# Performance work log

Measured on AMD Instinct MI355X. Metric: run time of the kernel, lower is better.

Reference implementation:

```python
import jax, jax.numpy as jnp
import numpy as np

BS, N, L, H, E, W, K = 32, 512, 4096, 256, 64, 8, 9
NE = 2048            # edges per graph
CIN = H + 2 * E + W  # pc1 input channels
CS = K // 2          # center slice start
LC = L - (K - 1)     # valid-conv output length
EPS = 1e-5


def setup_inputs() -> dict:
    key = jax.random.key(0)
    ks = jax.random.split(key, 12)
    s = 0.05
    d = {}
    d["x"] = jax.random.normal(ks[0], (BS, N, H), jnp.float32)
    d["edge_feat"] = jax.random.normal(ks[1], (BS, NE, E), jnp.float32)
    d["walk_nodes"] = jax.random.randint(ks[2], (BS, L), 0, N - 1)
    d["walk_edges"] = jax.random.randint(ks[3], (BS, L - 1), 0, NE)
    d["encodings"] = jax.random.normal(ks[4], (BS, W, L), jnp.float32)
    d["ln_g"] = jnp.ones((H,), jnp.float32)
    d["ln_b"] = jnp.zeros((H,), jnp.float32)
    d["pc1_w"] = jax.random.normal(ks[5], (2 * H, CIN), jnp.float32) * s
    d["pc1_b"] = jnp.zeros((2 * H,), jnp.float32)
    d["dc_w"] = jax.random.normal(ks[6], (H, K), jnp.float32) * s
    d["bn_g"] = jnp.ones((H,), jnp.float32)
    d["bn_b"] = jnp.zeros((H,), jnp.float32)
    d["pc2_w"] = jax.random.normal(ks[7], (H, H), jnp.float32) * s
    d["pc2_b"] = jnp.zeros((H,), jnp.float32)
    d["mlp_w1"] = jax.random.normal(ks[8], (H, H), jnp.float32) * s
    d["bn2_g"] = jnp.ones((H,), jnp.float32)
    d["bn2_b"] = jnp.zeros((H,), jnp.float32)
    d["mlp_w2"] = jax.random.normal(ks[9], (H, H), jnp.float32) * s
    return d


def reference(x, edge_feat, walk_nodes, walk_edges, encodings,
              ln_g, ln_b, pc1_w, pc1_b, dc_w, bn_g, bn_b,
              pc2_w, pc2_b, mlp_w1, bn2_g, bn2_b, mlp_w2):
    # LayerNorm over hidden dim
    mu = x.mean(-1, keepdims=True)
    var = x.var(-1, keepdims=True)
    xn = (x - mu) * jax.lax.rsqrt(var + EPS) * ln_g + ln_b

    vn = xn[:, 0]  # [BS, H]

    # gather walk node features: x[batch, walk_nodes+1] -> [BS, H, L]
    xg = jnp.take_along_axis(xn, (walk_nodes + 1)[:, :, None], axis=1)
    xg = xg.transpose(0, 2, 1)

    # gather walk edge features -> [BS, E, L-1], pad to in/out channels of len L
    we = jnp.take_along_axis(edge_feat, walk_edges[:, :, None], axis=1).transpose(0, 2, 1)
    pad = jnp.zeros((BS, E, 1), xg.dtype)
    we_i = jnp.concatenate([pad, we], axis=2)
    we_o = jnp.concatenate([we, pad], axis=2)

    h = jnp.concatenate([xg, we_i, we_o, encodings], axis=1)  # [BS, CIN, L]

    # pointwise conv 1 + GLU
    h = jnp.einsum('oc,bcl->bol', pc1_w, h) + pc1_b[None, :, None]
    out, gate = jnp.split(h, 2, axis=1)
    h = out * jax.nn.sigmoid(gate)  # [BS, H, L]

    # depthwise conv, VALID -> [BS, H, LC]
    h = jax.lax.conv_general_dilated(
        h, dc_w[:, None, :], window_strides=(1,), padding='VALID',
        feature_group_count=H, dimension_numbers=('NCH', 'OIH', 'NCH'))

    # BatchNorm1d (training mode, biased var over batch+length)
    m = h.mean((0, 2))
    v = h.var((0, 2))
    h = (h - m[None, :, None]) * jax.lax.rsqrt(v + EPS)[None, :, None] \
        * bn_g[None, :, None] + bn_b[None, :, None]

    # Swish + pointwise conv 2
    h = h * jax.nn.sigmoid(h)
    h = jnp.einsum('oc,bcl->bol', pc2_w, h) + pc2_b[None, :, None]
    h = h.transpose(0, 2, 1)  # [BS, LC, H]

    # scatter_mean over center nodes into n-1 real-node slots
    center = jax.lax.dynamic_slice_in_dim(walk_nodes, CS, LC, axis=1)  # [BS, LC]
    flat_idx = (center + jnp.arange(BS, dtype=center.dtype)[:, None] * (N - 1)).reshape(-1)
    sums = jax.ops.segment_sum(h.reshape(BS * LC, H), flat_idx, num_segments=BS * (N - 1))
    cnt = jax.ops.segment_sum(jnp.ones((BS * LC,), h.dtype), flat_idx, num_segments=BS * (N - 1))
    node_out = (sums / jnp.maximum(cnt, 1.0)[:, None]).reshape(BS, N - 1, H)

    # virtual node MLP: Linear -> BN -> ReLU -> Linear
    z = (vn + node_out.sum(1)) @ mlp_w1.T
    m2 = z.mean(0)
    v2 = z.var(0)
    z = (z - m2) * jax.lax.rsqrt(v2 + EPS) * bn2_g + bn2_b
    z = jax.nn.relu(z) @ mlp_w2.T
    vn_out = z[:, None]  # [BS, 1, H]

    return jnp.concatenate([vn_out, node_out + vn_out], axis=1)  # [BS, N, H]
```

## Files before the change

### kernel.cpp

```cpp
#include <hip/hip_runtime.h>
#include <hip/hip_bf16.h>

typedef __hip_bfloat16 bf16;
typedef __attribute__((ext_vector_type(8))) short short8v;
typedef __attribute__((ext_vector_type(4))) float f32x4;

#define BS 32
#define NN 512
#define LL 4096
#define HH 256
#define EE 64
#define WW 8
#define KK 9
#define NE 2048
#define CIN 392
#define KP 416
#define FS 424
#define FS2 264
#define LC 4088
#define NM1 511
#define CR 128
#define K2M 128
#define K5M 64

__device__ __forceinline__ float b2f(bf16 v) { return __bfloat162float(v); }
__device__ __forceinline__ float bfr(unsigned short u) {
    union { unsigned int i; float f; } cv; cv.i = ((unsigned int)u) << 16; return cv.f;
}
__device__ __forceinline__ unsigned short f2b(float v) {
    return __builtin_bit_cast(unsigned short, __float2bfloat16(v));
}
__device__ __forceinline__ unsigned int pack2(float a, float b) {
    return (unsigned int)f2b(a) | ((unsigned int)f2b(b) << 16);
}
__device__ __forceinline__ float sigm(float x) {
    return __builtin_amdgcn_rcpf(1.f + __expf(-x));
}

__global__ void k0_all(const float* __restrict__ pc1w, const float* __restrict__ pc2w,
                       const float* __restrict__ edge, unsigned short* __restrict__ wb,
                       unsigned short* __restrict__ w2b, unsigned short* __restrict__ eb) {
    size_t i = (size_t)blockIdx.x * 256 + threadIdx.x;
    eb[i] = f2b(edge[i]);
    if (i < (size_t)512 * KP) {
        int row = (int)(i / KP), c = (int)(i % KP);
        wb[i] = (c < CIN) ? f2b(pc1w[(size_t)row * CIN + c]) : 0;
    }
    if (i < (size_t)HH * HH) w2b[i] = f2b(pc2w[i]);
}

__global__ void k1_layernorm(const float* __restrict__ x, const float* __restrict__ ln_g,
                             const float* __restrict__ ln_b, unsigned short* __restrict__ xnb,
                             float* __restrict__ acc) {
    int b = blockIdx.y, n = blockIdx.x, t = threadIdx.x;
    size_t base = ((size_t)(b * NN + n)) * HH;
    float v = x[base + t];
    __shared__ float s1[4], s2[4], mv[2];
    float a = v, q = v * v;
    #pragma unroll
    for (int o = 32; o > 0; o >>= 1) { a += __shfl_down(a, o, 64); q += __shfl_down(q, o, 64); }
    if ((t & 63) == 0) { s1[t >> 6] = a; s2[t >> 6] = q; }
    __syncthreads();
    if (t == 0) {
        float sa = s1[0] + s1[1] + s1[2] + s1[3];
        float sq = s2[0] + s2[1] + s2[2] + s2[3];
        float mean = sa * (1.0f / 256.0f);
        float var = sq * (1.0f / 256.0f) - mean * mean;
        mv[0] = mean; mv[1] = rsqrtf(var + 1e-5f);
    }
    __syncthreads();
    float outv = (v - mv[0]) * mv[1] * ln_g[t] + ln_b[t];
    xnb[base + t] = f2b(outv);
    if (n == 0) acc[b * HH + t] = outv;
}

__global__ void kb1_count(const int* __restrict__ wn, int* __restrict__ count) {
    int b = blockIdx.y, l = blockIdx.x * 256 + threadIdx.x;
    if (l < LC) atomicAdd(&count[b * NM1 + wn[b * LL + l + (KK / 2)]], 1);
}

__global__ void kb2_scan(const int* __restrict__ count, int* __restrict__ offs,
                         int* __restrict__ cursor) {
    int b = blockIdx.x, t = threadIdx.x;
    __shared__ int ps[256];
    int c0 = (2 * t < NM1)     ? count[b * NM1 + 2 * t]     : 0;
    int c1 = (2 * t + 1 < NM1) ? count[b * NM1 + 2 * t + 1] : 0;
    int pair = c0 + c1;
    ps[t] = pair;
    __syncthreads();
    for (int o = 1; o < 256; o <<= 1) {
        int add = (t >= o) ? ps[t - o] : 0;
        __syncthreads();
        ps[t] += add;
        __syncthreads();
    }
    int ex = ps[t] - pair;
    offs[b * 512 + 2 * t] = ex;
    offs[b * 512 + 2 * t + 1] = ex + c0;
    if (2 * t < NM1)     cursor[b * NM1 + 2 * t]     = ex;
    if (2 * t + 1 < NM1) cursor[b * NM1 + 2 * t + 1] = ex + c0;
}

__global__ void kb3_fill(const int* __restrict__ wn, int* __restrict__ cursor,
                         int* __restrict__ bins) {
    int b = blockIdx.y, l = blockIdx.x * 256 + threadIdx.x;
    if (l < LC) {
        int c = wn[b * LL + l + (KK / 2)];
        int slot = atomicAdd(&cursor[b * NM1 + c], 1);
        bins[b * LC + slot] = l;
    }
}

__global__ void __launch_bounds__(512, 2)
k2_mfma(const unsigned short* __restrict__ xnb, const unsigned short* __restrict__ edgeb,
        const int* __restrict__ wn, const int* __restrict__ we,
        const float* __restrict__ enc, const unsigned short* __restrict__ wb,
        const float* __restrict__ pc1_b, unsigned short* __restrict__ h1) {
    __shared__ __align__(16) unsigned short smem[K2M * FS];
    __shared__ int rown[K2M], ein[K2M], eout[K2M];
    int b = blockIdx.y, l0 = blockIdx.x * K2M, t = threadIdx.x;
    int lane = t & 63, wv = t >> 6;
    int l15 = lane & 15, lr = (lane >> 4) & 3, koff = lr * 8;
    int isG = wv >> 2;
    int c0 = isG * 256 + (wv & 3) * 64;
    const unsigned short* wr = wb + ((size_t)(c0 + l15)) * KP + koff;

    short8v b0[4], b1[4];
    #pragma unroll
    for (int n = 0; n < 4; ++n) b0[n] = *(const short8v*)(wr + (size_t)n * 16 * KP);

    if (t < K2M) {
        int l = l0 + t;
        rown[t] = wn[b * LL + l] + 1;
        ein[t]  = (l > 0)      ? we[b * (LL - 1) + l - 1] : -1;
        eout[t] = (l < LL - 1) ? we[b * (LL - 1) + l]     : -1;
    }
    __syncthreads();

    for (int i = t; i < K2M * 32; i += 512) {
        int r = i >> 5, c = (i & 31) * 8;
        *(uint4*)&smem[r * FS + c] =
            *(const uint4*)(xnb + ((size_t)(b * NN + rown[r])) * HH + c);
    }
    for (int i = t; i < K2M * 16; i += 512) {
        int r = i >> 4, q = i & 15;
        int idx = (q < 8) ? ein[r] : eout[r];
        uint4 v = {0u, 0u, 0u, 0u};
        if (idx >= 0)
            v = *(const uint4*)(edgeb + ((size_t)(b * NE + idx)) * EE + (q & 7) * 8);
        *(uint4*)&smem[r * FS + HH + q * 8] = v;
    }
    for (int i = t; i < K2M * 5; i += 512) {
        int r = i / 5, q = i % 5;
        uint4 v = {0u, 0u, 0u, 0u};
        if (q == 0) {
            const float* ep = enc + (size_t)b * WW * LL + (l0 + r);
            v.x = pack2(ep[0], ep[LL]);          v.y = pack2(ep[2 * LL], ep[3 * LL]);
            v.z = pack2(ep[4 * LL], ep[5 * LL]); v.w = pack2(ep[6 * LL], ep[7 * LL]);
        }
        *(uint4*)&smem[r * FS + (HH + 2 * EE) + q * 8] = v;
    }
    __syncthreads();

    f32x4 acc[8][4];
    #pragma unroll
    for (int m = 0; m < 8; ++m)
        #pragma unroll
        for (int n = 0; n < 4; ++n) acc[m][n] = (f32x4){0.f, 0.f, 0.f, 0.f};

    const unsigned short* arow = &smem[l15 * FS + koff];

    #pragma unroll 1
    for (int p = 0; p < 6; ++p) {
        int kk = 2 * p;
        #pragma unroll
        for (int n = 0; n < 4; ++n)
            b1[n] = *(const short8v*)(wr + (size_t)n * 16 * KP + (kk + 1) * 32);
        {
            short8v a[8];
            #pragma unroll
            for (int m = 0; m < 8; ++m)
                a[m] = *(const short8v*)(arow + (size_t)m * 16 * FS + kk * 32);
            #pragma unroll
            for (int m = 0; m < 8; ++m)
                #pragma unroll
                for (int n = 0; n < 4; ++n)
                    acc[m][n] = __builtin_amdgcn_mfma_f32_16x16x32_bf16(a[m], b0[n], acc[m][n], 0, 0, 0);
        }
        #pragma unroll
        for (int n = 0; n < 4; ++n)
            b0[n] = *(const short8v*)(wr + (size_t)n * 16 * KP + (kk + 2) * 32);
        {
            short8v a[8];
            #pragma unroll
            for (int m = 0; m < 8; ++m)
                a[m] = *(const short8v*)(arow + (size_t)m * 16 * FS + (kk + 1) * 32);
            #pragma unroll
            for (int m = 0; m < 8; ++m)
                #pragma unroll
                for (int n = 0; n < 4; ++n)
                    acc[m][n] = __builtin_amdgcn_mfma_f32_16x16x32_bf16(a[m], b1[n], acc[m][n], 0, 0, 0);
        }
    }
    {
        short8v a[8];
        #pragma unroll
        for (int m = 0; m < 8; ++m)
            a[m] = *(const short8v*)(arow + (size_t)m * 16 * FS + 12 * 32);
        #pragma unroll
        for (int m = 0; m < 8; ++m)
            #pragma unroll
            for (int n = 0; n < 4; ++n)
                acc[m][n] = __builtin_amdgcn_mfma_f32_16x16x32_bf16(a[m], b0[n], acc[m][n], 0, 0, 0);
    }

    float bias[4];
    #pragma unroll
    for (int n = 0; n < 4; ++n) bias[n] = pc1_b[c0 + n * 16 + l15];

    __syncthreads();
    unsigned short* glu = smem;
    int cb = (wv & 3) * 64 + l15;
    if (isG) {
        #pragma unroll
        for (int m = 0; m < 8; ++m)
            #pragma unroll
            for (int n = 0; n < 4; ++n)
                #pragma unroll
                for (int r = 0; r < 4; ++r) {
                    int pos = m * 16 + lr * 4 + r;
                    glu[pos * FS2 + cb + n * 16] = f2b(acc[m][n][r] + bias[n]);
                }
    }
    __syncthreads();
    if (!isG) {
        #pragma unroll
        for (int m = 0; m < 8; ++m)
            #pragma unroll
            for (int n = 0; n < 4; ++n)
                #pragma unroll
                for (int r = 0; r < 4; ++r) {
                    int pos = m * 16 + lr * 4 + r;
                    float g = bfr(glu[pos * FS2 + cb + n * 16]);
                    float o = acc[m][n][r] + bias[n];
                    glu[pos * FS2 + cb + n * 16] = f2b(o * sigm(g));
                }
    }
    __syncthreads();
    for (int i = t; i < K2M * 32; i += 512) {
        int r = i >> 5, c = (i & 31) * 8;
        *(uint4*)(h1 + ((size_t)(b * LL) + l0 + r) * HH + c) = *(const uint4*)&glu[r * FS2 + c];
    }
}

__global__ void k3f_conv_stats(const unsigned short* __restrict__ h1, const float* __restrict__ dc_w,
                               unsigned short* __restrict__ h2, float* __restrict__ bnsum,
                               float* __restrict__ bnsumsq) {
    __shared__ float sr[4][HH], qr[4][HH];
    int b = blockIdx.y, l0 = blockIdx.x * CR, t = threadIdx.x;
    int g = t >> 6, c4 = (t & 63) * 4;
    int rows_all = min(CR, LC - l0);
    int r0 = g * (CR / 4);
    int r1 = min(r0 + CR / 4, rows_all);

    float wk[4][KK];
    #pragma unroll
    for (int j = 0; j < 4; ++j)
        #pragma unroll
        for (int k = 0; k < KK; ++k) wk[j][k] = dc_w[(c4 + j) * KK + k];

    float s[4] = {0.f, 0.f, 0.f, 0.f}, q[4] = {0.f, 0.f, 0.f, 0.f};
    if (r0 < r1) {
        const unsigned short* src = h1 + ((size_t)b * LL + l0 + r0) * HH + c4;
        float w[KK][4];
        float nxt[4];
        #pragma unroll
        for (int k = 0; k < KK - 1; ++k) {
            uint2 v = *(const uint2*)(src + (size_t)k * HH);
            w[k][0] = bfr((unsigned short)(v.x & 0xffffu)); w[k][1] = bfr((unsigned short)(v.x >> 16));
            w[k][2] = bfr((unsigned short)(v.y & 0xffffu)); w[k][3] = bfr((unsigned short)(v.y >> 16));
        }
        {
            uint2 v = *(const uint2*)(src + (size_t)(KK - 1) * HH);
            nxt[0] = bfr((unsigned short)(v.x & 0xffffu)); nxt[1] = bfr((unsigned short)(v.x >> 16));
            nxt[2] = bfr((unsigned short)(v.y & 0xffffu)); nxt[3] = bfr((unsigned short)(v.y >> 16));
        }
        for (int i = r0; i < r1; ++i) {
            #pragma unroll
            for (int j = 0; j < 4; ++j) w[KK - 1][j] = nxt[j];
            if (i + 1 < r1) {
                uint2 v = *(const uint2*)(src + (size_t)(i - r0 + KK) * HH);
                nxt[0] = bfr((unsigned short)(v.x & 0xffffu)); nxt[1] = bfr((unsigned short)(v.x >> 16));
                nxt[2] = bfr((unsigned short)(v.y & 0xffffu)); nxt[3] = bfr((unsigned short)(v.y >> 16));
            }
            float o[4];
            #pragma unroll
            for (int j = 0; j < 4; ++j) {
                float v = 0.f;
                #pragma unroll
                for (int k = 0; k < KK; ++k) v += w[k][j] * wk[j][k];
                o[j] = v;
                s[j] += v; q[j] += v * v;
            }
            uint2 ov;
            ov.x = pack2(o[0], o[1]); ov.y = pack2(o[2], o[3]);
            *(uint2*)(h2 + ((size_t)b * LC + l0 + i) * HH + c4) = ov;
            #pragma unroll
            for (int k = 0; k < KK - 1; ++k)
                #pragma unroll
                for (int j = 0; j < 4; ++j) w[k][j] = w[k + 1][j];
        }
    }
    #pragma unroll
    for (int j = 0; j < 4; ++j) { sr[g][c4 + j] = s[j]; qr[g][c4 + j] = q[j]; }
    __syncthreads();
    float ss = sr[0][t] + sr[1][t] + sr[2][t] + sr[3][t];
    float qq = qr[0][t] + qr[1][t] + qr[2][t] + qr[3][t];
    atomicAdd(&bnsum[t], ss);
    atomicAdd(&bnsumsq[t], qq);
}

__global__ void k4b_finalize(const float* __restrict__ bnsum, const float* __restrict__ bnsumsq,
                             const float* __restrict__ bn_g, const float* __restrict__ bn_b,
                             float* __restrict__ bnscale, float* __restrict__ bnshift) {
    int c = threadIdx.x;
    const float M = (float)(BS * LC);
    float mean = bnsum[c] / M;
    float var = bnsumsq[c] / M - mean * mean;
    float rstd = rsqrtf(var + 1e-5f);
    float sc = rstd * bn_g[c];
    bnscale[c] = sc;
    bnshift[c] = bn_b[c] - mean * sc;
}

__global__ void __launch_bounds__(256, 3)
k5_mfma(const unsigned short* __restrict__ h2, const float* __restrict__ bnscale,
        const float* __restrict__ bnshift, const unsigned short* __restrict__ w2b,
        const float* __restrict__ pc2_b, unsigned short* __restrict__ h3) {
    __shared__ __align__(16) unsigned short smem[K5M * FS2];
    __shared__ float scl[HH], shl[HH];
    int b = blockIdx.y, l0 = blockIdx.x * K5M, t = threadIdx.x;
    int lane = t & 63, wv = t >> 6;
    int l15 = lane & 15, lr = (lane >> 4) & 3, koff = lr * 8;
    int c0 = wv * 64;
    const unsigned short* wrow = w2b + ((size_t)(c0 + l15)) * HH + koff;

    short8v b0[4], b1[4];
    #pragma unroll
    for (int n = 0; n < 4; ++n) b0[n] = *(const short8v*)(wrow + (size_t)n * 16 * HH);

    scl[t] = bnscale[t];
    shl[t] = bnshift[t];
    __syncthreads();

    for (int i = t; i < K5M * 32; i += 256) {
        int r = i >> 5, c = (i & 31) * 8;
        int l = l0 + r;
        uint4 out = {0u, 0u, 0u, 0u};
        if (l < LC) {
            uint4 v = *(const uint4*)(h2 + ((size_t)b * LC + l) * HH + c);
            unsigned int vv[4] = {v.x, v.y, v.z, v.w};
            unsigned int oo[4];
            #pragma unroll
            for (int j = 0; j < 4; ++j) {
                float f0 = bfr((unsigned short)(vv[j] & 0xffffu));
                float f1 = bfr((unsigned short)(vv[j] >> 16));
                float a0 = f0 * scl[c + 2 * j]     + shl[c + 2 * j];
                float a1 = f1 * scl[c + 2 * j + 1] + shl[c + 2 * j + 1];
                a0 = a0 * sigm(a0);
                a1 = a1 * sigm(a1);
                oo[j] = pack2(a0, a1);
            }
            out.x = oo[0]; out.y = oo[1]; out.z = oo[2]; out.w = oo[3];
        }
        *(uint4*)&smem[r * FS2 + c] = out;
    }
    __syncthreads();

    f32x4 acc[4][4];
    #pragma unroll
    for (int m = 0; m < 4; ++m)
        #pragma unroll
        for (int n = 0; n < 4; ++n) acc[m][n] = (f32x4){0.f, 0.f, 0.f, 0.f};

    const unsigned short* arow = &smem[l15 * FS2 + koff];

    #pragma unroll 1
    for (int p = 0; p < 4; ++p) {
        int kk = 2 * p;
        #pragma unroll
        for (int n = 0; n < 4; ++n)
            b1[n] = *(const short8v*)(wrow + (size_t)n * 16 * HH + (kk + 1) * 32);
        {
            short8v a[4];
            #pragma unroll
            for (int m = 0; m < 4; ++m)
                a[m] = *(const short8v*)(arow + (size_t)m * 16 * FS2 + kk * 32);
            #pragma unroll
            for (int m = 0; m < 4; ++m)
                #pragma unroll
                for (int n = 0; n < 4; ++n)
                    acc[m][n] = __builtin_amdgcn_mfma_f32_16x16x32_bf16(a[m], b0[n], acc[m][n], 0, 0, 0);
        }
        if (p < 3) {
            #pragma unroll
            for (int n = 0; n < 4; ++n)
                b0[n] = *(const short8v*)(wrow + (size_t)n * 16 * HH + (kk + 2) * 32);
        }
        {
            short8v a[4];
            #pragma unroll
            for (int m = 0; m < 4; ++m)
                a[m] = *(const short8v*)(arow + (size_t)m * 16 * FS2 + (kk + 1) * 32);
            #pragma unroll
            for (int m = 0; m < 4; ++m)
                #pragma unroll
                for (int n = 0; n < 4; ++n)
                    acc[m][n] = __builtin_amdgcn_mfma_f32_16x16x32_bf16(a[m], b1[n], acc[m][n], 0, 0, 0);
        }
    }

    int chb = c0 + l15;
    float bias[4];
    #pragma unroll
    for (int n = 0; n < 4; ++n) bias[n] = pc2_b[chb + n * 16];

    __syncthreads();
    #pragma unroll
    for (int m = 0; m < 4; ++m)
        #pragma unroll
        for (int n = 0; n < 4; ++n)
            #pragma unroll
            for (int r = 0; r < 4; ++r) {
                int pos = m * 16 + lr * 4 + r;
                smem[pos * FS2 + chb + n * 16] = f2b(acc[m][n][r] + bias[n]);
            }
    __syncthreads();
    for (int i = t; i < K5M * 32; i += 256) {
        int r = i >> 5, c = (i & 31) * 8;
        int l = l0 + r;
        if (l < LC)
            *(uint4*)(h3 + ((size_t)b * LC + l) * HH + c) = *(const uint4*)&smem[r * FS2 + c];
    }
}

__global__ void k6_gather(const unsigned short* __restrict__ h3, const int* __restrict__ offs,
                          const int* __restrict__ bins, float* __restrict__ node_out) {
    int bn = blockIdx.x;
    int b = bn / NM1, n = bn % NM1, t = threadIdx.x;
    int s = offs[b * 512 + n], e = offs[b * 512 + n + 1];
    float sum = 0.f;
    for (int i = s; i < e; ++i) {
        int l = bins[b * LC + i];
        sum += bfr(h3[((size_t)b * LC + l) * HH + t]);
    }
    float inv = 1.f / (float)max(e - s, 1);
    node_out[(size_t)bn * HH + t] = sum * inv;
}

__global__ void k6b_accsum(const float* __restrict__ node_out, float* __restrict__ acc) {
    int b = blockIdx.y, g = blockIdx.x, t = threadIdx.x;
    int n0 = g * 32, n1 = min(n0 + 32, NM1);
    float s = 0.f;
    for (int n = n0; n < n1; ++n) s += node_out[((size_t)b * NM1 + n) * HH + t];
    atomicAdd(&acc[b * HH + t], s);
}

__global__ void k7_mlp1(const float* __restrict__ acc, const float* __restrict__ w1,
                        float* __restrict__ z) {
    int b = blockIdx.x, t = threadIdx.x;
    __shared__ float a[HH];
    a[t] = acc[b * HH + t];
    __syncthreads();
    const float* w = w1 + (size_t)t * HH;
    float s = 0.f;
    for (int c = 0; c < HH; ++c) s += w[c] * a[c];
    z[b * HH + t] = s;
}

__global__ void k8_bn2(float* __restrict__ z, const float* __restrict__ g2,
                       const float* __restrict__ b2v) {
    int t = threadIdx.x;
    float vals[BS];
    float m = 0.f, q = 0.f;
    for (int b = 0; b < BS; ++b) {
        float v = z[b * HH + t];
        vals[b] = v; m += v; q += v * v;
    }
    m *= (1.0f / BS);
    q = q * (1.0f / BS) - m * m;
    float rstd = rsqrtf(q + 1e-5f);
    float sc = rstd * g2[t];
    float sh = b2v[t] - m * sc;
    for (int b = 0; b < BS; ++b) z[b * HH + t] = fmaxf(vals[b] * sc + sh, 0.f);
}

__global__ void k9_mlp2(const float* __restrict__ z, const float* __restrict__ w2,
                        float* __restrict__ vnout) {
    int b = blockIdx.x, t = threadIdx.x;
    __shared__ float a[HH];
    a[t] = z[b * HH + t];
    __syncthreads();
    const float* w = w2 + (size_t)t * HH;
    float s = 0.f;
    for (int c = 0; c < HH; ++c) s += w[c] * a[c];
    vnout[b * HH + t] = s;
}

__global__ void k10_out(const float* __restrict__ vnout, const float* __restrict__ node_out,
                        float* __restrict__ out) {
    int bn = blockIdx.x;
    int b = bn >> 9, n = bn & (NN - 1), t = threadIdx.x;
    float vo = vnout[b * HH + t];
    float v = (n == 0) ? vo : node_out[((size_t)b * NM1 + (n - 1)) * HH + t] + vo;
    out[(size_t)bn * HH + t] = v;
}

extern "C" void kernel_launch(void* const* d_in, const int* in_sizes, int n_in,
                              void* d_out, int out_size, void* d_ws, size_t ws_size,
                              hipStream_t stream) {
    const float* x     = (const float*)d_in[0];
    const float* edge  = (const float*)d_in[1];
    const int*   wn    = (const int*)d_in[2];
    const int*   we    = (const int*)d_in[3];
    const float* enc   = (const float*)d_in[4];
    const float* ln_g  = (const float*)d_in[5];
    const float* ln_b  = (const float*)d_in[6];
    const float* pc1_w = (const float*)d_in[7];
    const float* pc1_b = (const float*)d_in[8];
    const float* dc_w  = (const float*)d_in[9];
    const float* bn_g  = (const float*)d_in[10];
    const float* bn_b  = (const float*)d_in[11];
    const float* pc2_w = (const float*)d_in[12];
    const float* pc2_b = (const float*)d_in[13];
    const float* w1    = (const float*)d_in[14];
    const float* g2    = (const float*)d_in[15];
    const float* b2v   = (const float*)d_in[16];
    const float* w2    = (const float*)d_in[17];

    char* ws = (char*)d_ws;
    unsigned short* xnb   = (unsigned short*)(ws + 0);
    unsigned short* wbf   = (unsigned short*)(ws + 8388608);
    unsigned short* h1    = (unsigned short*)(ws + 8814592);
    unsigned short* h3    = h1;
    unsigned short* h2    = (unsigned short*)(ws + 75923456);
    float* node_out = (float*)(ws + 142901248);
    unsigned short* edgeb = (unsigned short*)(ws + 142901248);
    int*   count   = (int*)(ws + 159645696);
    float* bnsum   = (float*)(ws + 159711104);
    float* bnsumsq = (float*)(ws + 159712128);
    float* acc     = (float*)(ws + 159713152);
    float* bnscale = (float*)(ws + 159745920);
    float* bnshift = (float*)(ws + 159746944);
    float* z       = (float*)(ws + 159747968);
    float* vnout   = (float*)(ws + 159780736);
    unsigned short* w2b = (unsigned short*)(ws + 159813504);
    int*   offs    = (int*)(ws + 159944576);
    int*   cursor  = (int*)(ws + 160010112);
    int*   bins    = (int*)(ws + 160075520);

    hipMemsetAsync(ws + 159645696, 0, 67456, stream);

    k0_all<<<(BS * NE * EE) / 256, 256, 0, stream>>>(pc1_w, pc2_w, edge, wbf, w2b, edgeb);
    k1_layernorm<<<dim3(NN, BS), 256, 0, stream>>>(x, ln_g, ln_b, xnb, acc);
    kb1_count<<<dim3(16, BS), 256, 0, stream>>>(wn, count);
    kb2_scan<<<BS, 256, 0, stream>>>(count, offs, cursor);
    kb3_fill<<<dim3(16, BS), 256, 0, stream>>>(wn, cursor, bins);
    k2_mfma<<<dim3(LL / K2M, BS), 512, 0, stream>>>(xnb, edgeb, wn, we, enc, wbf, pc1_b, h1);
    k3f_conv_stats<<<dim3((LC + CR - 1) / CR, BS), 256, 0, stream>>>(h1, dc_w, h2, bnsum, bnsumsq);
    k4b_finalize<<<1, 256, 0, stream>>>(bnsum, bnsumsq, bn_g, bn_b, bnscale, bnshift);
    k5_mfma<<<dim3((LC + K5M - 1) / K5M, BS), 256, 0, stream>>>(h2, bnscale, bnshift, w2b, pc2_b, h3);
    k6_gather<<<BS * NM1, 256, 0, stream>>>(h3, offs, bins, node_out);
    k6b_accsum<<<dim3(16, BS), 256, 0, stream>>>(node_out, acc);
    k7_mlp1<<<BS, 256, 0, stream>>>(acc, w1, z);
    k8_bn2<<<1, 256, 0, stream>>>(z, g2, b2v);
    k9_mlp2<<<BS, 256, 0, stream>>>(z, w2, vnout);
    k10_out<<<BS * NN, 256, 0, stream>>>(vnout, node_out, (float*)d_out);
}
```

Baseline: 297.0 us.

## Fuse binning kernels into one LDS kernel and restructure GLU GEMM tiling

The three binning kernels (count, scan, fill) are merged into a single per-batch kernel that does its histogram and cursor atomics in shared memory, which removes two launches and the global count/cursor buffers and shrinks the memset. The pc1 GEMM kernel now uses 64-row tiles and 256 threads, and each wave computes both the output and gate columns for the same 64 channels. The GLU can then be applied directly from registers, with no round trip through shared memory and no extra barrier. The cost is twice as many blocks, each loading its own copy of the weight B-fragments, and more accumulator registers per wave. The binning kernel now runs on only 32 blocks.

Result: faster. 290.7 us (-2.1%).

```diff
diff --git a/kernel.cpp b/kernel.cpp
--- a/kernel.cpp
+++ b/kernel.cpp
@@ -20,7 +20,7 @@
 #define LC 4088
 #define NM1 511
 #define CR 128
-#define K2M 128
+#define K2M 64
 #define K5M 64
 
 __device__ __forceinline__ float b2f(bf16 v) { return __bfloat162float(v); }
@@ -74,17 +74,19 @@
     if (n == 0) acc[b * HH + t] = outv;
 }
 
-__global__ void kb1_count(const int* __restrict__ wn, int* __restrict__ count) {
-    int b = blockIdx.y, l = blockIdx.x * 256 + threadIdx.x;
-    if (l < LC) atomicAdd(&count[b * NM1 + wn[b * LL + l + (KK / 2)]], 1);
-}
-
-__global__ void kb2_scan(const int* __restrict__ count, int* __restrict__ offs,
-                         int* __restrict__ cursor) {
+__global__ void kb_all(const int* __restrict__ wn, int* __restrict__ offs,
+                       int* __restrict__ bins) {
+    __shared__ int cnt[NM1];
+    __shared__ int cur[NM1];
+    __shared__ int ps[256];
     int b = blockIdx.x, t = threadIdx.x;
-    __shared__ int ps[256];
-    int c0 = (2 * t < NM1)     ? count[b * NM1 + 2 * t]     : 0;
-    int c1 = (2 * t + 1 < NM1) ? count[b * NM1 + 2 * t + 1] : 0;
+    for (int i = t; i < NM1; i += 256) cnt[i] = 0;
+    __syncthreads();
+    for (int l = t; l < LC; l += 256)
+        atomicAdd(&cnt[wn[b * LL + l + (KK / 2)]], 1);
+    __syncthreads();
+    int c0 = (2 * t < NM1)     ? cnt[2 * t]     : 0;
+    int c1 = (2 * t + 1 < NM1) ? cnt[2 * t + 1] : 0;
     int pair = c0 + c1;
     ps[t] = pair;
     __syncthreads();
@@ -97,21 +99,17 @@
     int ex = ps[t] - pair;
     offs[b * 512 + 2 * t] = ex;
     offs[b * 512 + 2 * t + 1] = ex + c0;
-    if (2 * t < NM1)     cursor[b * NM1 + 2 * t]     = ex;
-    if (2 * t + 1 < NM1) cursor[b * NM1 + 2 * t + 1] = ex + c0;
-}
-
-__global__ void kb3_fill(const int* __restrict__ wn, int* __restrict__ cursor,
-                         int* __restrict__ bins) {
-    int b = blockIdx.y, l = blockIdx.x * 256 + threadIdx.x;
-    if (l < LC) {
+    if (2 * t < NM1)     cur[2 * t]     = ex;
+    if (2 * t + 1 < NM1) cur[2 * t + 1] = ex + c0;
+    __syncthreads();
+    for (int l = t; l < LC; l += 256) {
         int c = wn[b * LL + l + (KK / 2)];
-        int slot = atomicAdd(&cursor[b * NM1 + c], 1);
+        int slot = atomicAdd(&cur[c], 1);
         bins[b * LC + slot] = l;
     }
 }
 
-__global__ void __launch_bounds__(512, 2)
+__global__ void __launch_bounds__(256, 2)
 k2_mfma(const unsigned short* __restrict__ xnb, const unsigned short* __restrict__ edgeb,
         const int* __restrict__ wn, const int* __restrict__ we,
         const float* __restrict__ enc, const unsigned short* __restrict__ wb,
@@ -121,13 +119,16 @@
     int b = blockIdx.y, l0 = blockIdx.x * K2M, t = threadIdx.x;
     int lane = t & 63, wv = t >> 6;
     int l15 = lane & 15, lr = (lane >> 4) & 3, koff = lr * 8;
-    int isG = wv >> 2;
-    int c0 = isG * 256 + (wv & 3) * 64;
-    const unsigned short* wr = wb + ((size_t)(c0 + l15)) * KP + koff;
-
-    short8v b0[4], b1[4];
-    #pragma unroll
-    for (int n = 0; n < 4; ++n) b0[n] = *(const short8v*)(wr + (size_t)n * 16 * KP);
+    int c0 = wv * 64;
+    const unsigned short* wrO = wb + ((size_t)(c0 + l15)) * KP + koff;
+    const unsigned short* wrG = wb + ((size_t)(HH + c0 + l15)) * KP + koff;
+
+    short8v bo0[4], bg0[4], bo1[4], bg1[4];
+    #pragma unroll
+    for (int n = 0; n < 4; ++n) {
+        bo0[n] = *(const short8v*)(wrO + (size_t)n * 16 * KP);
+        bg0[n] = *(const short8v*)(wrG + (size_t)n * 16 * KP);
+    }
 
     if (t < K2M) {
         int l = l0 + t;
@@ -137,12 +138,12 @@
     }
     __syncthreads();
 
-    for (int i = t; i < K2M * 32; i += 512) {
+    for (int i = t; i < K2M * 32; i += 256) {
         int r = i >> 5, c = (i & 31) * 8;
         *(uint4*)&smem[r * FS + c] =
             *(const uint4*)(xnb + ((size_t)(b * NN + rown[r])) * HH + c);
     }
-    for (int i = t; i < K2M * 16; i += 512) {
+    for (int i = t; i < K2M * 16; i += 256) {
         int r = i >> 4, q = i & 15;
         int idx = (q < 8) ? ein[r] : eout[r];
         uint4 v = {0u, 0u, 0u, 0u};
@@ -150,7 +151,7 @@
             v = *(const uint4*)(edgeb + ((size_t)(b * NE + idx)) * EE + (q & 7) * 8);
         *(uint4*)&smem[r * FS + HH + q * 8] = v;
     }
-    for (int i = t; i < K2M * 5; i += 512) {
+    for (int i = t; i < K2M * 5; i += 256) {
         int r = i / 5, q = i % 5;
         uint4 v = {0u, 0u, 0u, 0u};
         if (q == 0) {
@@ -162,11 +163,11 @@
     }
     __syncthreads();
 
-    f32x4 acc[8][4];
-    #pragma unroll
-    for (int m = 0; m < 8; ++m)
-        #pragma unroll
-        for (int n = 0; n < 4; ++n) acc[m][n] = (f32x4){0.f, 0.f, 0.f, 0.f};
+    f32x4 acc[4][8];
+    #pragma unroll
+    for (int m = 0; m < 4; ++m)
+        #pragma unroll
+        for (int n = 0; n < 8; ++n) acc[m][n] = (f32x4){0.f, 0.f, 0.f, 0.f};
 
     const unsigned short* arow = &smem[l15 * FS + koff];
 
@@ -174,80 +175,79 @@
     for (int p = 0; p < 6; ++p) {
         int kk = 2 * p;
         #pragma unroll
+        for (int n = 0; n < 4; ++n) {
+            bo1[n] = *(const short8v*)(wrO + (size_t)n * 16 * KP + (kk + 1) * 32);
+            bg1[n] = *(const short8v*)(wrG + (size_t)n * 16 * KP + (kk + 1) * 32);
+        }
+        {
+            short8v a[4];
+            #pragma unroll
+            for (int m = 0; m < 4; ++m)
+                a[m] = *(const short8v*)(arow + (size_t)m * 16 * FS + kk * 32);
+            #pragma unroll
+            for (int m = 0; m < 4; ++m)
+                #pragma unroll
+                for (int n = 0; n < 4; ++n) {
+                    acc[m][n]     = __builtin_amdgcn_mfma_f32_16x16x32_bf16(a[m], bo0[n], acc[m][n], 0, 0, 0);
+                    acc[m][n + 4] = __builtin_amdgcn_mfma_f32_16x16x32_bf16(a[m], bg0[n], acc[m][n + 4], 0, 0, 0);
+                }
+        }
+        #pragma unroll
+        for (int n = 0; n < 4; ++n) {
+            bo0[n] = *(const short8v*)(wrO + (size_t)n * 16 * KP + (kk + 2) * 32);
+            bg0[n] = *(const short8v*)(wrG + (size_t)n * 16 * KP + (kk + 2) * 32);
+        }
+        {
+            short8v a[4];
+            #pragma unroll
+            for (int m = 0; m < 4; ++m)
+                a[m] = *(const short8v*)(arow + (size_t)m * 16 * FS + (kk + 1) * 32);
+            #pragma unroll
+            for (int m = 0; m < 4; ++m)
+                #pragma unroll
+                for (int n = 0; n < 4; ++n) {
+                    acc[m][n]     = __builtin_amdgcn_mfma_f32_16x16x32_bf16(a[m], bo1[n], acc[m][n], 0, 0, 0);
+                    acc[m][n + 4] = __builtin_amdgcn_mfma_f32_16x16x32_bf16(a[m], bg1[n], acc[m][n + 4], 0, 0, 0);
+                }
+        }
+    }
+    {
+        short8v a[4];
+        #pragma unroll
+        for (int m = 0; m < 4; ++m)
+            a[m] = *(const short8v*)(arow + (size_t)m * 16 * FS + 12 * 32);
+        #pragma unroll
+        for (int m = 0; m < 4; ++m)
+            #pragma unroll
+            for (int n = 0; n < 4; ++n) {
+                acc[m][n]     = __builtin_amdgcn_mfma_f32_16x16x32_bf16(a[m], bo0[n], acc[m][n], 0, 0, 0);
+                acc[m][n + 4] = __builtin_amdgcn_mfma_f32_16x16x32_bf16(a[m], bg0[n], acc[m][n + 4], 0, 0, 0);
+            }
+    }
+
+    float biasO[4], biasG[4];
+    #pragma unroll
+    for (int n = 0; n < 4; ++n) {
+        biasO[n] = pc1_b[c0 + n * 16 + l15];
+        biasG[n] = pc1_b[HH + c0 + n * 16 + l15];
+    }
+
+    __syncthreads();
+    unsigned short* glu = smem;
+    int cb = c0 + l15;
+    #pragma unroll
+    for (int m = 0; m < 4; ++m)
+        #pragma unroll
         for (int n = 0; n < 4; ++n)
-            b1[n] = *(const short8v*)(wr + (size_t)n * 16 * KP + (kk + 1) * 32);
-        {
-            short8v a[8];
-            #pragma unroll
-            for (int m = 0; m < 8; ++m)
-                a[m] = *(const short8v*)(arow + (size_t)m * 16 * FS + kk * 32);
-            #pragma unroll
-            for (int m = 0; m < 8; ++m)
-                #pragma unroll
-                for (int n = 0; n < 4; ++n)
-                    acc[m][n] = __builtin_amdgcn_mfma_f32_16x16x32_bf16(a[m], b0[n], acc[m][n], 0, 0, 0);
-        }
-        #pragma unroll
-        for (int n = 0; n < 4; ++n)
-            b0[n] = *(const short8v*)(wr + (size_t)n * 16 * KP + (kk + 2) * 32);
-        {
-            short8v a[8];
-            #pragma unroll
-            for (int m = 0; m < 8; ++m)
-                a[m] = *(const short8v*)(arow + (size_t)m * 16 * FS + (kk + 1) * 32);
-            #pragma unroll
-            for (int m = 0; m < 8; ++m)
-                #pragma unroll
-                for (int n = 0; n < 4; ++n)
-                    acc[m][n] = __builtin_amdgcn_mfma_f32_16x16x32_bf16(a[m], b1[n], acc[m][n], 0, 0, 0);
-        }
-    }
-    {
-        short8v a[8];
-        #pragma unroll
-        for (int m = 0; m < 8; ++m)
-            a[m] = *(const short8v*)(arow + (size_t)m * 16 * FS + 12 * 32);
-        #pragma unroll
-        for (int m = 0; m < 8; ++m)
-            #pragma unroll
-            for (int n = 0; n < 4; ++n)
-                acc[m][n] = __builtin_amdgcn_mfma_f32_16x16x32_bf16(a[m], b0[n], acc[m][n], 0, 0, 0);
-    }
-
-    float bias[4];
-    #pragma unroll
-    for (int n = 0; n < 4; ++n) bias[n] = pc1_b[c0 + n * 16 + l15];
-
-    __syncthreads();
-    unsigned short* glu = smem;
-    int cb = (wv & 3) * 64 + l15;
-    if (isG) {
-        #pragma unroll
-        for (int m = 0; m < 8; ++m)
-            #pragma unroll
-            for (int n = 0; n < 4; ++n)
-                #pragma unroll
-                for (int r = 0; r < 4; ++r) {
-                    int pos = m * 16 + lr * 4 + r;
-                    glu[pos * FS2 + cb + n * 16] = f2b(acc[m][n][r] + bias[n]);
-                }
-    }
-    __syncthreads();
-    if (!isG) {
-        #pragma unroll
-        for (int m = 0; m < 8; ++m)
-            #pragma unroll
-            for (int n = 0; n < 4; ++n)
-                #pragma unroll
-                for (int r = 0; r < 4; ++r) {
-                    int pos = m * 16 + lr * 4 + r;
-                    float g = bfr(glu[pos * FS2 + cb + n * 16]);
-                    float o = acc[m][n][r] + bias[n];
-                    glu[pos * FS2 + cb + n * 16] = f2b(o * sigm(g));
-                }
-    }
-    __syncthreads();
-    for (int i = t; i < K2M * 32; i += 512) {
+            #pragma unroll
+            for (int r = 0; r < 4; ++r) {
+                int pos = m * 16 + lr * 4 + r;
+                float o = acc[m][n][r] + biasO[n];
+                float g = acc[m][n + 4][r] + biasG[n];
+                glu[pos * FS2 + cb + n * 16] = f2b(o * sigm(g));
+            }
+    __syncthreads();
+    for (int i = t; i < K2M * 32; i += 256) {
         int r = i >> 5, c = (i & 31) * 8;
         *(uint4*)(h1 + ((size_t)(b * LL) + l0 + r) * HH + c) = *(const uint4*)&glu[r * FS2 + c];
     }
@@ -546,7 +546,6 @@
     unsigned short* h2    = (unsigned short*)(ws + 75923456);
     float* node_out = (float*)(ws + 142901248);
     unsigned short* edgeb = (unsigned short*)(ws + 142901248);
-    int*   count   = (int*)(ws + 159645696);
     float* bnsum   = (float*)(ws + 159711104);
     float* bnsumsq = (float*)(ws + 159712128);
     float* acc     = (float*)(ws + 159713152);
@@ -556,17 +555,14 @@
     float* vnout   = (float*)(ws + 159780736);
     unsigned short* w2b = (unsigned short*)(ws + 159813504);
     int*   offs    = (int*)(ws + 159944576);
-    int*   cursor  = (int*)(ws + 160010112);
     int*   bins    = (int*)(ws + 160075520);
 
-    hipMemsetAsync(ws + 159645696, 0, 67456, stream);
+    hipMemsetAsync(ws + 159711104, 0, 2048, stream);
 
     k0_all<<<(BS * NE * EE) / 256, 256, 0, stream>>>(pc1_w, pc2_w, edge, wbf, w2b, edgeb);
     k1_layernorm<<<dim3(NN, BS), 256, 0, stream>>>(x, ln_g, ln_b, xnb, acc);
-    kb1_count<<<dim3(16, BS), 256, 0, stream>>>(wn, count);
-    kb2_scan<<<BS, 256, 0, stream>>>(count, offs, cursor);
-    kb3_fill<<<dim3(16, BS), 256, 0, stream>>>(wn, cursor, bins);
-    k2_mfma<<<dim3(LL / K2M, BS), 512, 0, stream>>>(xnb, edgeb, wn, we, enc, wbf, pc1_b, h1);
+    kb_all<<<BS, 256, 0, stream>>>(wn, offs, bins);
+    k2_mfma<<<dim3(LL / K2M, BS), 256, 0, stream>>>(xnb, edgeb, wn, we, enc, wbf, pc1_b, h1);
     k3f_conv_stats<<<dim3((LC + CR - 1) / CR, BS), 256, 0, stream>>>(h1, dc_w, h2, bnsum, bnsumsq);
     k4b_finalize<<<1, 256, 0, stream>>>(bnsum, bnsumsq, bn_g, bn_b, bnscale, bnshift);
     k5_mfma<<<dim3((LC + K5M - 1) / K5M, BS), 256, 0, stream>>>(h2, bnscale, bnshift, w2b, pc2_b, h3);
```
